# Optimization experiments

Hardware: AMD Instinct MI355X
Metric: run time of the kernel (lower is better)

Reference implementation:

```python
import jax, jax.numpy as jnp
import numpy as np
from jax import lax

GAMMA = 0.99
LAM = 0.95
CLIP_PARAM = 0.2
VALUE_LOSS_COEF = 0.5
ENTROPY_COEF = 0.01
EPS = 1e-09

B, T = 4096, 2048


def setup_inputs() -> dict:
    key = jax.random.key(0)
    ks = jax.random.split(key, 6)
    rewards = jax.random.normal(ks[0], (B, T), dtype=jnp.float32)
    values = jax.random.normal(ks[1], (B, T + 1), dtype=jnp.float32)
    ref_probs = jax.random.uniform(ks[2], (B, T), dtype=jnp.float32)
    old_probs = jax.random.uniform(ks[3], (B, T), dtype=jnp.float32)
    curr_probs = jax.random.uniform(ks[4], (B, T), dtype=jnp.float32)
    # episode-continuation masks: mostly 1, occasional 0 (episode boundary)
    masks = (jax.random.uniform(ks[5], (B, T)) > 0.02).astype(jnp.float32)
    return {"rewards": rewards, "values": values, "ref_probs": ref_probs,
            "old_probs": old_probs, "curr_probs": curr_probs, "masks": masks}


def compute_gae(rewards, values, masks, gamma, lam):
    # single fused reverse scan over time; per-step state is (B,)
    def step(carry, xs):
        r, v, v_next, m = xs
        delta = r + gamma * v_next * m - v
        adv = delta + gamma * lam * m * carry
        return adv, adv

    xs = (rewards.T, values[:, :-1].T, values[:, 1:].T, masks.T)  # each (T, B)
    _, advs = lax.scan(step, jnp.zeros(rewards.shape[0], rewards.dtype), xs, reverse=True)
    advantages = advs.T  # (B, T)
    returns = advantages + values[:, :-1]
    return advantages, returns


def reference(rewards, values, ref_probs, old_probs, curr_probs, masks):
    advantages, returns = compute_gae(rewards, values, masks, GAMMA, LAM)
    # torch .std() is unbiased (ddof=1)
    advantages = (advantages - advantages.mean()) / (advantages.std(ddof=1) + EPS)
    ratios = curr_probs / (old_probs + EPS)
    surr1 = ratios * advantages
    surr2 = jnp.clip(ratios, 1.0 - CLIP_PARAM, 1.0 + CLIP_PARAM) * advantages
    ppo_loss = -jnp.minimum(surr1, surr2).mean()
    value_loss = jnp.mean((returns - values[:, :-1]) ** 2)
    entropy_loss = -jnp.mean(curr_probs * jnp.log(curr_probs + EPS))
    total_loss = ppo_loss + VALUE_LOSS_COEF * value_loss + ENTROPY_COEF * entropy_loss
    return (total_loss, ppo_loss, VALUE_LOSS_COEF * value_loss, ENTROPY_COEF * entropy_loss)
```

## Files before the change

kernel.cpp:

```cpp
#include <hip/hip_runtime.h>
#include <math.h>


#define GAMMA     0.99f
#define LAM       0.95f
#define CLIP_LO   0.8f
#define CLIP_HI   1.2f
#define EPSF      1e-9f

constexpr int BB = 4096;
constexpr int TT = 2048;
constexpr long long NN = (long long)BB * TT;
constexpr int PPO_BLOCKS = 2048;

struct Stats { float mean; float inv; double sum2; };
static constexpr size_t GAE_PART_OFF = 64;
static constexpr size_t PPO_PART_OFF = 64 + 4096 * sizeof(float2);
static constexpr size_t ADV_OFF      = PPO_PART_OFF + 2048 * sizeof(float2);

__global__ __launch_bounds__(256) void gae_kernel(
    const float* __restrict__ rewards,
    const float* __restrict__ values,
    const float* __restrict__ masks,
    float* __restrict__ adv_out,
    float2* __restrict__ partials)
{
    const int row = blockIdx.x;
    const int tid = threadIdx.x;
    const int t0  = tid * 8;

    const float* rrow = rewards + (size_t)row * TT;
    const float* mrow = masks   + (size_t)row * TT;
    const float* vrow = values  + (size_t)row * (TT + 1);

    float4 r0 = *(const float4*)(rrow + t0);
    float4 r1 = *(const float4*)(rrow + t0 + 4);
    float4 m0 = *(const float4*)(mrow + t0);
    float4 m1 = *(const float4*)(mrow + t0 + 4);
    float r[8] = {r0.x, r0.y, r0.z, r0.w, r1.x, r1.y, r1.z, r1.w};
    float m[8] = {m0.x, m0.y, m0.z, m0.w, m1.x, m1.y, m1.z, m1.w};
    float v[9];
#pragma unroll
    for (int j = 0; j < 9; ++j) v[j] = vrow[t0 + j];

    float delta[8], c[8];
#pragma unroll
    for (int j = 0; j < 8; ++j) {
        delta[j] = r[j] + GAMMA * v[j + 1] * m[j] - v[j];
        c[j]     = (GAMMA * LAM) * m[j];
    }

    float la[8], S[8];
    la[7] = delta[7];
    S[7]  = c[7];
#pragma unroll
    for (int j = 6; j >= 0; --j) {
        la[j] = delta[j] + c[j] * la[j + 1];
        S[j]  = c[j] * S[j + 1];
    }

    __shared__ float sA[2][256];
    __shared__ float sB[2][256];
    int buf = 0;
    sA[0][tid] = S[0];
    sB[0][tid] = la[0];
    __syncthreads();
#pragma unroll
    for (int d = 1; d < 256; d <<= 1) {
        float A = sA[buf][tid], Bv = sB[buf][tid];
        if (tid + d < 256) {
            float A2 = sA[buf][tid + d], B2 = sB[buf][tid + d];
            Bv = Bv + A * B2;
            A  = A * A2;
        }
        buf ^= 1;
        sA[buf][tid] = A;
        sB[buf][tid] = Bv;
        __syncthreads();
    }
    float carry = (tid < 255) ? sB[buf][tid + 1] : 0.0f;

    float a[8], s1 = 0.f, s2 = 0.f;
#pragma unroll
    for (int j = 0; j < 8; ++j) {
        a[j] = la[j] + S[j] * carry;
        s1 += a[j];
        s2 += a[j] * a[j];
    }
    float4 o0 = {a[0], a[1], a[2], a[3]};
    float4 o1 = {a[4], a[5], a[6], a[7]};
    *(float4*)(adv_out + (size_t)row * TT + t0)     = o0;
    *(float4*)(adv_out + (size_t)row * TT + t0 + 4) = o1;

#pragma unroll
    for (int off = 32; off > 0; off >>= 1) {
        s1 += __shfl_down(s1, off, 64);
        s2 += __shfl_down(s2, off, 64);
    }
    __shared__ float w1[4], w2[4];
    const int wave = tid >> 6, lane = tid & 63;
    if (lane == 0) { w1[wave] = s1; w2[wave] = s2; }
    __syncthreads();
    if (tid == 0) {
        float2 p = {w1[0] + w1[1] + w1[2] + w1[3],
                    w2[0] + w2[1] + w2[2] + w2[3]};
        partials[row] = p;
    }
}

__global__ __launch_bounds__(256) void finalize_stats(
    const float2* __restrict__ gp, Stats* __restrict__ stats)
{
    const int tid = threadIdx.x;
    __shared__ double l1[256], l2[256];
    double s1 = 0.0, s2 = 0.0;
    for (int i = tid; i < BB; i += 256) {
        float2 p = gp[i];
        s1 += (double)p.x;
        s2 += (double)p.y;
    }
    l1[tid] = s1; l2[tid] = s2;
    __syncthreads();
    for (int st = 128; st > 0; st >>= 1) {
        if (tid < st) { l1[tid] += l1[tid + st]; l2[tid] += l2[tid + st]; }
        __syncthreads();
    }
    if (tid == 0) {
        double S1 = l1[0], S2 = l2[0];
        double mean = S1 / (double)NN;
        double var  = (S2 - S1 * S1 / (double)NN) / (double)(NN - 1);
        stats->mean = (float)mean;
        stats->inv  = (float)(1.0 / (sqrt(var) + 1e-9));
        stats->sum2 = S2;
    }
}

__global__ __launch_bounds__(256) void ppo_kernel(
    const float* __restrict__ adv,
    const float* __restrict__ oldp,
    const float* __restrict__ currp,
    const Stats* __restrict__ stats,
    float2* __restrict__ partials)
{
    const float mean = stats->mean;
    const float inv  = stats->inv;
    const long long n4 = NN / 4;

    const float4* a4 = (const float4*)adv;
    const float4* o4 = (const float4*)oldp;
    const float4* c4 = (const float4*)currp;

    float sm = 0.f, se = 0.f;
    long long idx    = (long long)blockIdx.x * blockDim.x + threadIdx.x;
    long long stride = (long long)gridDim.x * blockDim.x;
    for (long long i = idx; i < n4; i += stride) {
        float4 a = a4[i], o = o4[i], c = c4[i];
        float av[4] = {a.x, a.y, a.z, a.w};
        float ov[4] = {o.x, o.y, o.z, o.w};
        float cv[4] = {c.x, c.y, c.z, c.w};
#pragma unroll
        for (int j = 0; j < 4; ++j) {
            float an    = (av[j] - mean) * inv;
            float ratio = cv[j] / (ov[j] + EPSF);
            float rc    = fminf(fmaxf(ratio, CLIP_LO), CLIP_HI);
            sm += fminf(ratio * an, rc * an);
            se += cv[j] * __logf(cv[j] + EPSF);
        }
    }

#pragma unroll
    for (int off = 32; off > 0; off >>= 1) {
        sm += __shfl_down(sm, off, 64);
        se += __shfl_down(se, off, 64);
    }
    __shared__ float w1[4], w2[4];
    const int wave = threadIdx.x >> 6, lane = threadIdx.x & 63;
    if (lane == 0) { w1[wave] = sm; w2[wave] = se; }
    __syncthreads();
    if (threadIdx.x == 0) {
        float2 p = {w1[0] + w1[1] + w1[2] + w1[3],
                    w2[0] + w2[1] + w2[2] + w2[3]};
        partials[blockIdx.x] = p;
    }
}

__global__ __launch_bounds__(256) void finalize_out(
    const float2* __restrict__ pp,
    const Stats* __restrict__ stats,
    float* __restrict__ out)
{
    const int tid = threadIdx.x;
    __shared__ double l1[256], l2[256];
    double s1 = 0.0, s2 = 0.0;
    for (int i = tid; i < PPO_BLOCKS; i += 256) {
        float2 p = pp[i];
        s1 += (double)p.x;
        s2 += (double)p.y;
    }
    l1[tid] = s1; l2[tid] = s2;
    __syncthreads();
    for (int st = 128; st > 0; st >>= 1) {
        if (tid < st) { l1[tid] += l1[tid + st]; l2[tid] += l2[tid + st]; }
        __syncthreads();
    }
    if (tid == 0) {
        double invN = 1.0 / (double)NN;
        double vl   = 0.5  * (stats->sum2 * invN);
        double ppo  = -(l1[0] * invN);
        double ent  = -0.01 * (l2[0] * invN);
        out[0] = (float)(ppo + vl + ent);
        out[1] = (float)ppo;
        out[2] = (float)vl;
        out[3] = (float)ent;
    }
}

extern "C" void kernel_launch(void* const* d_in, const int* in_sizes, int n_in,
                              void* d_out, int out_size, void* d_ws, size_t ws_size,
                              hipStream_t stream) {
    const float* rewards = (const float*)d_in[0];
    const float* values  = (const float*)d_in[1];
    const float* oldp    = (const float*)d_in[3];
    const float* currp   = (const float*)d_in[4];
    const float* masks   = (const float*)d_in[5];

    Stats*  stats = (Stats*)d_ws;
    float2* gaep  = (float2*)((char*)d_ws + GAE_PART_OFF);
    float2* ppop  = (float2*)((char*)d_ws + PPO_PART_OFF);
    float*  advws = (float*)((char*)d_ws + ADV_OFF);
    float*  out   = (float*)d_out;

    gae_kernel<<<BB, 256, 0, stream>>>(rewards, values, masks, advws, gaep);
    finalize_stats<<<1, 256, 0, stream>>>(gaep, stats);
    ppo_kernel<<<PPO_BLOCKS, 256, 0, stream>>>(advws, oldp, currp, stats, ppop);
    finalize_out<<<1, 256, 0, stream>>>(ppop, stats, out);
}
```

Measured before the change: 209.6 us.

## Use wave-shuffle scan in GAE, stage values in LDS, unroll PPO loads

```diff
diff --git a/kernel.cpp b/kernel.cpp
--- a/kernel.cpp
+++ b/kernel.cpp
@@ -18,16 +18,22 @@
 static constexpr size_t PPO_PART_OFF = 64 + 4096 * sizeof(float2);
 static constexpr size_t ADV_OFF      = PPO_PART_OFF + 2048 * sizeof(float2);
 
-__global__ __launch_bounds__(256) void gae_kernel(
+__global__ __launch_bounds__(256, 8) void gae_kernel(
     const float* __restrict__ rewards,
     const float* __restrict__ values,
     const float* __restrict__ masks,
     float* __restrict__ adv_out,
     float2* __restrict__ partials)
 {
-    const int row = blockIdx.x;
-    const int tid = threadIdx.x;
-    const int t0  = tid * 8;
+    const int row  = blockIdx.x;
+    const int tid  = threadIdx.x;
+    const int lane = tid & 63;
+    const int wave = tid >> 6;
+    const int t0   = tid * 8;
+
+    __shared__ float  lv[2052];
+    __shared__ float2 wT[4];
+    __shared__ float  wr1[4], wr2[4];
 
     const float* rrow = rewards + (size_t)row * TT;
     const float* mrow = masks   + (size_t)row * TT;
@@ -37,11 +43,17 @@
     float4 r1 = *(const float4*)(rrow + t0 + 4);
     float4 m0 = *(const float4*)(mrow + t0);
     float4 m1 = *(const float4*)(mrow + t0 + 4);
+
+#pragma unroll
+    for (int k = 0; k < 8; ++k) lv[tid + 256 * k] = vrow[tid + 256 * k];
+    if (tid == 0) lv[2048] = vrow[2048];
+    __syncthreads();
+
     float r[8] = {r0.x, r0.y, r0.z, r0.w, r1.x, r1.y, r1.z, r1.w};
     float m[8] = {m0.x, m0.y, m0.z, m0.w, m1.x, m1.y, m1.z, m1.w};
     float v[9];
 #pragma unroll
-    for (int j = 0; j < 9; ++j) v[j] = vrow[t0 + j];
+    for (int j = 0; j < 9; ++j) v[j] = lv[t0 + j];
 
     float delta[8], c[8];
 #pragma unroll
@@ -59,26 +71,25 @@
         S[j]  = c[j] * S[j + 1];
     }
 
-    __shared__ float sA[2][256];
-    __shared__ float sB[2][256];
-    int buf = 0;
-    sA[0][tid] = S[0];
-    sB[0][tid] = la[0];
-    __syncthreads();
-#pragma unroll
-    for (int d = 1; d < 256; d <<= 1) {
-        float A = sA[buf][tid], Bv = sB[buf][tid];
-        if (tid + d < 256) {
-            float A2 = sA[buf][tid + d], B2 = sB[buf][tid + d];
+    float A = S[0], Bv = la[0];
+#pragma unroll
+    for (int d = 1; d < 64; d <<= 1) {
+        float A2 = __shfl_down(A,  d, 64);
+        float B2 = __shfl_down(Bv, d, 64);
+        if (lane + d < 64) {
             Bv = Bv + A * B2;
             A  = A * A2;
         }
-        buf ^= 1;
-        sA[buf][tid] = A;
-        sB[buf][tid] = Bv;
-        __syncthreads();
-    }
-    float carry = (tid < 255) ? sB[buf][tid + 1] : 0.0f;
+    }
+    if (lane == 0) wT[wave] = make_float2(A, Bv);
+    __syncthreads();
+    float C = 0.0f;
+    for (int ww = 3; ww > wave; --ww)
+        C = wT[ww].y + wT[ww].x * C;
+
+    float A1 = __shfl_down(A,  1, 64);
+    float B1 = __shfl_down(Bv, 1, 64);
+    float carry = (lane < 63) ? (B1 + A1 * C) : C;
 
     float a[8], s1 = 0.f, s2 = 0.f;
 #pragma unroll
@@ -97,13 +108,11 @@
         s1 += __shfl_down(s1, off, 64);
         s2 += __shfl_down(s2, off, 64);
     }
-    __shared__ float w1[4], w2[4];
-    const int wave = tid >> 6, lane = tid & 63;
-    if (lane == 0) { w1[wave] = s1; w2[wave] = s2; }
-    __syncthreads();
-    if (tid == 0) {
-        float2 p = {w1[0] + w1[1] + w1[2] + w1[3],
-                    w2[0] + w2[1] + w2[2] + w2[3]};
+    if (lane == 0) { wr1[wave] = s1; wr2[wave] = s2; }
+    __syncthreads();
+    if (tid == 0) {
+        float2 p = {wr1[0] + wr1[1] + wr1[2] + wr1[3],
+                    wr2[0] + wr2[1] + wr2[2] + wr2[3]};
         partials[row] = p;
     }
 }
@@ -135,7 +144,7 @@
     }
 }
 
-__global__ __launch_bounds__(256) void ppo_kernel(
+__global__ __launch_bounds__(256, 4) void ppo_kernel(
     const float* __restrict__ adv,
     const float* __restrict__ oldp,
     const float* __restrict__ currp,
@@ -144,24 +153,32 @@
 {
     const float mean = stats->mean;
     const float inv  = stats->inv;
-    const long long n4 = NN / 4;
+    const int tid = threadIdx.x;
+
+    const long long base   = (long long)blockIdx.x * 256 + tid;
+    const long long stride = (long long)PPO_BLOCKS * 256;
 
     const float4* a4 = (const float4*)adv;
     const float4* o4 = (const float4*)oldp;
     const float4* c4 = (const float4*)currp;
 
+    float4 Af[4], Of[4], Cf[4];
+#pragma unroll
+    for (int k = 0; k < 4; ++k) {
+        long long i = base + (long long)k * stride;
+        Af[k] = a4[i]; Of[k] = o4[i]; Cf[k] = c4[i];
+    }
+
     float sm = 0.f, se = 0.f;
-    long long idx    = (long long)blockIdx.x * blockDim.x + threadIdx.x;
-    long long stride = (long long)gridDim.x * blockDim.x;
-    for (long long i = idx; i < n4; i += stride) {
-        float4 a = a4[i], o = o4[i], c = c4[i];
-        float av[4] = {a.x, a.y, a.z, a.w};
-        float ov[4] = {o.x, o.y, o.z, o.w};
-        float cv[4] = {c.x, c.y, c.z, c.w};
+#pragma unroll
+    for (int k = 0; k < 4; ++k) {
+        float av[4] = {Af[k].x, Af[k].y, Af[k].z, Af[k].w};
+        float ov[4] = {Of[k].x, Of[k].y, Of[k].z, Of[k].w};
+        float cv[4] = {Cf[k].x, Cf[k].y, Cf[k].z, Cf[k].w};
 #pragma unroll
         for (int j = 0; j < 4; ++j) {
             float an    = (av[j] - mean) * inv;
-            float ratio = cv[j] / (ov[j] + EPSF);
+            float ratio = cv[j] * __builtin_amdgcn_rcpf(ov[j] + EPSF);
             float rc    = fminf(fmaxf(ratio, CLIP_LO), CLIP_HI);
             sm += fminf(ratio * an, rc * an);
             se += cv[j] * __logf(cv[j] + EPSF);
@@ -174,10 +191,10 @@
         se += __shfl_down(se, off, 64);
     }
     __shared__ float w1[4], w2[4];
-    const int wave = threadIdx.x >> 6, lane = threadIdx.x & 63;
+    const int wave = tid >> 6, lane = tid & 63;
     if (lane == 0) { w1[wave] = sm; w2[wave] = se; }
     __syncthreads();
-    if (threadIdx.x == 0) {
+    if (tid == 0) {
         float2 p = {w1[0] + w1[1] + w1[2] + w1[3],
                     w2[0] + w2[1] + w2[2] + w2[3]};
         partials[blockIdx.x] = p;
```

Result: no change. 210.7 us (+0.5%).
